# Optimization experiments

Hardware: AMD Instinct MI355X
Metric: run time of the kernel (lower is better)

## Reference

```python
import jax, jax.numpy as jnp
import numpy as np

B, S, D = 2, 4096, 512   # batch, seq_len, input_dim
W, H = 256, 4            # memory width (d_model), attention heads
DH = W // H              # per-head depth


def _dense(x, w, b):
    return x @ w + b


def setup_inputs() -> dict:
    key = jax.random.key(0)
    ks = jax.random.split(key, 24)
    def w(k, shape):
        return jax.random.normal(k, shape, dtype=jnp.float32) * 0.02
    inp = {
        "x": jax.random.normal(ks[0], (B, S, D), dtype=jnp.float32),
        # outer q/k/v projections D -> W
        "qp_w": w(ks[1], (D, W)), "qp_b": jnp.zeros((W,), jnp.float32),
        "kp_w": w(ks[2], (D, W)), "kp_b": jnp.zeros((W,), jnp.float32),
        "vp_w": w(ks[3], (D, W)), "vp_b": jnp.zeros((W,), jnp.float32),
        # MHA internal projections W -> W
        "wq_w": w(ks[4], (W, W)), "wq_b": jnp.zeros((W,), jnp.float32),
        "wk_w": w(ks[5], (W, W)), "wk_b": jnp.zeros((W,), jnp.float32),
        "wv_w": w(ks[6], (W, W)), "wv_b": jnp.zeros((W,), jnp.float32),
        "wo_w": w(ks[7], (W, W)), "wo_b": jnp.zeros((W,), jnp.float32),
        # deep MLP memory (depth=2, gelu) + its output proj W -> W
        "m0_w": w(ks[8], (W, W)), "m0_b": jnp.zeros((W,), jnp.float32),
        "m1_w": w(ks[9], (W, W)), "m1_b": jnp.zeros((W,), jnp.float32),
        "mo_w": w(ks[10], (W, W)), "mo_b": jnp.zeros((W,), jnp.float32),
        # final output projection W -> D
        "op_w": w(ks[11], (W, D)), "op_b": jnp.zeros((D,), jnp.float32),
    }
    return inp


def reference(x, qp_w, qp_b, kp_w, kp_b, vp_w, vp_b,
              wq_w, wq_b, wk_w, wk_b, wv_w, wv_b, wo_w, wo_b,
              m0_w, m0_b, m1_w, m1_b, mo_w, mo_b, op_w, op_b):
    # outer projections (D -> W)
    q0 = _dense(x, qp_w, qp_b)
    k0 = _dense(x, kp_w, kp_b)
    v0 = _dense(x, vp_w, vp_b)
    # MHA internal projections (W -> W)
    q = _dense(q0, wq_w, wq_b)
    k = _dense(k0, wk_w, wk_b)
    v = _dense(v0, wv_w, wv_b)
    # split heads: [B,S,W] -> [B,H,S,DH]
    def split(t):
        return t.reshape(B, S, H, DH).transpose(0, 2, 1, 3)
    qh, kh, vh = split(q), split(k), split(v)
    scores = jnp.einsum('bhqd,bhkd->bhqk', qh, kh) / jnp.sqrt(jnp.float32(DH))
    attn = jax.nn.softmax(scores, axis=-1)
    ctx = jnp.einsum('bhqk,bhkd->bhqd', attn, vh)
    ctx = ctx.transpose(0, 2, 1, 3).reshape(B, S, W)
    retrieved = _dense(ctx, wo_w, wo_b)
    # deep MLP memory (exact gelu, matching keras 'gelu')
    h = jax.nn.gelu(_dense(retrieved, m0_w, m0_b), approximate=False)
    h = jax.nn.gelu(_dense(h, m1_w, m1_b), approximate=False)
    mem = _dense(h, mo_w, mo_b)
    # final projection + residual
    out = _dense(mem, op_w, op_b) + x
    return out
```

## Files before the change

### kernel.cpp

```cpp
#include <hip/hip_runtime.h>
#include <cstdint>
#include <cstddef>


#define GAS(p) ((const __attribute__((address_space(1))) void*)(p))
#define LAS(p) ((__attribute__((address_space(3))) void*)(p))

typedef __attribute__((ext_vector_type(8))) short bfrag;
typedef __attribute__((ext_vector_type(4))) float facc;
typedef __attribute__((ext_vector_type(16))) float facc16;
typedef uint16_t u16;

__device__ __forceinline__ u16 f2bf(float f) {
  uint32_t u = __float_as_uint(f);
  u += 0x7fffu + ((u >> 16) & 1u);
  return (u16)(u >> 16);
}
__device__ __forceinline__ float bf2f(u16 h) {
  return __uint_as_float((uint32_t)h << 16);
}
__device__ __forceinline__ float gelu_exact(float v) {
  return 0.5f * v * (1.f + erff(v * 0.70710678118654752440f));
}
__device__ __forceinline__ facc mfma16(bfrag a, bfrag b, facc c) {
  return __builtin_amdgcn_mfma_f32_16x16x32_bf16(a, b, c, 0, 0, 0);
}
__device__ __forceinline__ facc16 mfma32(bfrag a, bfrag b, facc16 c) {
  return __builtin_amdgcn_mfma_f32_32x32x16_bf16(a, b, c, 0, 0, 0);
}

union U4 { uint32_t w[4]; bfrag f; };

__device__ __forceinline__ bfrag lds_frag(const u16* lds, int row, int kk, int ln) {
  int kb  = (kk << 6) + ((ln >> 4) << 4);
  int off = (row << 7) + (kb ^ ((row & 7) << 4));
  return *(const bfrag*)((const char*)lds + off);
}
__device__ __forceinline__ bfrag lds_frag_rb(const u16* lds, int row, int bytecol) {
  int off = (row << 7) + (bytecol ^ ((row & 7) << 4));
  return *(const bfrag*)((const char*)lds + off);
}

template <int ROWS, int NW>
__device__ __forceinline__ void stage_tile(const u16* gbase, int ldK, u16* lds,
                                           int wv, int ln) {
#pragma unroll
  for (int i = 0; i < ROWS / 8 / NW; i++) {
    int seg = i * NW + wv;
    int row = (seg << 3) + (ln >> 3);
    int kb  = (ln & 7) << 4;
    const char* g = (const char*)(gbase + (size_t)row * ldK) +
                    (kb ^ ((row & 7) << 4));
    __builtin_amdgcn_global_load_lds(GAS(g), LAS(lds + (seg << 9)), 16, 0, 0);
  }
}

template <int EPI, int BN>
__global__ __launch_bounds__(256) void gemm_bt(
    const u16* __restrict__ A, const u16* __restrict__ Bt,
    const float* __restrict__ bias, const float* __restrict__ resid,
    u16* __restrict__ obf, float* __restrict__ of32,
    u16* __restrict__ qb, u16* __restrict__ kb2, u16* __restrict__ vb,
    int M, int N, int K) {
  const int t = threadIdx.x, wv = t >> 6, ln = t & 63;
  const int wr = wv >> 1, wc = wv & 1;
  const int m0 = blockIdx.y << 7, n0 = blockIdx.x * BN;
  constexpr int NJ = BN / 32;

  __shared__ __align__(16) u16 Al[128 * 64];
  __shared__ __align__(16) u16 Bl[BN * 64];

  facc acc[4][NJ];
#pragma unroll
  for (int i = 0; i < 4; i++)
#pragma unroll
    for (int j = 0; j < NJ; j++)
#pragma unroll
      for (int r = 0; r < 4; r++) acc[i][j][r] = 0.f;

  const u16* Ab = A + (size_t)m0 * K;
  const u16* Bb = Bt + (size_t)n0 * K;
  stage_tile<128, 4>(Ab, K, Al, wv, ln);
  stage_tile<BN, 4>(Bb, K, Bl, wv, ln);

  const int nk = K >> 6;
  for (int kt = 0; kt < nk; ++kt) {
    __syncthreads();
#pragma unroll
    for (int kk = 0; kk < 2; kk++) {
      bfrag av[4], bv[NJ];
#pragma unroll
      for (int i = 0; i < 4; i++)
        av[i] = lds_frag(Al, (wr << 6) + (i << 4) + (ln & 15), kk, ln);
#pragma unroll
      for (int j = 0; j < NJ; j++)
        bv[j] = lds_frag(Bl, wc * (BN / 2) + (j << 4) + (ln & 15), kk, ln);
      __builtin_amdgcn_s_setprio(1);
#pragma unroll
      for (int i = 0; i < 4; i++)
#pragma unroll
        for (int j = 0; j < NJ; j++)
          acc[i][j] = mfma16(av[i], bv[j], acc[i][j]);
      __builtin_amdgcn_s_setprio(0);
    }
    if (kt + 1 < nk) {
      __syncthreads();
      stage_tile<128, 4>(Ab + (kt + 1) * 64, K, Al, wv, ln);
      stage_tile<BN, 4>(Bb + (kt + 1) * 64, K, Bl, wv, ln);
    }
  }

  const int rb = (ln >> 4) << 2, cb = ln & 15;
#pragma unroll
  for (int i = 0; i < 4; i++) {
#pragma unroll
    for (int j = 0; j < NJ; j++) {
      const int col = n0 + wc * (BN / 2) + (j << 4) + cb;
      const float bcol = bias ? bias[col] : 0.f;
#pragma unroll
      for (int r = 0; r < 4; r++) {
        const int row = m0 + (wr << 6) + (i << 4) + rb + r;
        float val = acc[i][j][r] + bcol;
        if (EPI == 0) {
          obf[(size_t)row * N + col] = f2bf(val);
        } else if (EPI == 1) {
          obf[(size_t)row * N + col] = f2bf(gelu_exact(val));
        } else if (EPI == 2) {
          const int sec = col >> 8, cc = col & 255, h = cc >> 6, dh = cc & 63;
          const int b = row >> 12, s = row & 4095;
          const size_t idx = (((size_t)(b * 4 + h)) * 4096 + s) * 64 + dh;
          if (sec == 0) qb[idx] = f2bf(val * 0.18033688011112042f);
          else if (sec == 1) kb2[idx] = f2bf(val);
          else vb[idx] = f2bf(val);
        } else {
          of32[(size_t)row * N + col] = val + resid[(size_t)row * N + col];
        }
      }
    }
  }
}

__global__ __launch_bounds__(256) void wgemm5(
    const u16* __restrict__ wqkvT, const u16* __restrict__ owqkv,
    const u16* __restrict__ m0_t, const u16* __restrict__ wo_bf,
    const u16* __restrict__ opT, const u16* __restrict__ mo_bf,
    u16* __restrict__ Wqkv_t, u16* __restrict__ Wf1_t,
    u16* __restrict__ Wmo_t) {
  const int z = blockIdx.z;
  const u16 *A, *Bt; u16* out; int M, N, rowOff;
  if (z < 3)      { A = wqkvT + z * 65536; Bt = owqkv + z * 131072;
                    out = Wqkv_t; M = 256; N = 512; rowOff = z * 256; }
  else if (z == 3){ A = m0_t; Bt = wo_bf; out = Wf1_t; M = 256; N = 256; rowOff = 0; }
  else            { A = opT;  Bt = mo_bf; out = Wmo_t; M = 512; N = 256; rowOff = 0; }
  const int m0 = blockIdx.y << 7, n0 = blockIdx.x << 6;
  if (m0 >= M || n0 >= N) return;

  const int t = threadIdx.x, wv = t >> 6, ln = t & 63;
  const int wr = wv >> 1, wc = wv & 1;
  __shared__ __align__(16) u16 Al[128 * 64];
  __shared__ __align__(16) u16 Bl[64 * 64];

  facc acc[4][2];
#pragma unroll
  for (int i = 0; i < 4; i++)
#pragma unroll
    for (int j = 0; j < 2; j++)
#pragma unroll
      for (int r = 0; r < 4; r++) acc[i][j][r] = 0.f;

  const u16* Ab = A + (size_t)m0 * 256;
  const u16* Bb = Bt + (size_t)n0 * 256;
  stage_tile<128, 4>(Ab, 256, Al, wv, ln);
  stage_tile<64, 4>(Bb, 256, Bl, wv, ln);

  for (int kt = 0; kt < 4; ++kt) {
    __syncthreads();
#pragma unroll
    for (int kk = 0; kk < 2; kk++) {
      bfrag av[4], bv[2];
#pragma unroll
      for (int i = 0; i < 4; i++)
        av[i] = lds_frag(Al, (wr << 6) + (i << 4) + (ln & 15), kk, ln);
#pragma unroll
      for (int j = 0; j < 2; j++)
        bv[j] = lds_frag(Bl, wc * 32 + (j << 4) + (ln & 15), kk, ln);
#pragma unroll
      for (int i = 0; i < 4; i++)
#pragma unroll
        for (int j = 0; j < 2; j++)
          acc[i][j] = mfma16(av[i], bv[j], acc[i][j]);
    }
    if (kt + 1 < 4) {
      __syncthreads();
      stage_tile<128, 4>(Ab + (kt + 1) * 64, 256, Al, wv, ln);
      stage_tile<64, 4>(Bb + (kt + 1) * 64, 256, Bl, wv, ln);
    }
  }

  const int rb = (ln >> 4) << 2, cb = ln & 15;
#pragma unroll
  for (int i = 0; i < 4; i++)
#pragma unroll
    for (int j = 0; j < 2; j++) {
      const int col = n0 + wc * 32 + (j << 4) + cb;
#pragma unroll
      for (int r = 0; r < 4; r++) {
        const int row = m0 + (wr << 6) + (i << 4) + rb + r;
        out[(size_t)(rowOff + row) * N + col] = f2bf(acc[i][j][r]);
      }
    }
}

__global__ __launch_bounds__(128) void attn4(
    const u16* __restrict__ qg, const u16* __restrict__ kg,
    const u16* __restrict__ vtg, u16* __restrict__ Opart,
    float* __restrict__ lpart) {
  const int t = threadIdx.x, wv = t >> 6, ln = t & 63;
  const int l31 = ln & 31, lh = ln >> 5;
  const int qt = blockIdx.x, bh = blockIdx.y, kv = blockIdx.z;
  const int qbase = qt * 128 + wv * 64;
  const u16* Q  = qg + ((size_t)bh * 4096 + qbase) * 64;
  const u16* Kb = kg + ((size_t)bh * 4096 + kv * 1024) * 64;
  const u16* Vt = vtg + (size_t)bh * 64 * 4096 + kv * 1024;

  __shared__ __align__(16) u16 Klds[2][4096];
  __shared__ __align__(16) u16 Vlds[2][4096];

  bfrag qf[2][4];
#pragma unroll
  for (int qi = 0; qi < 2; qi++) {
    const u16* qp = Q + (size_t)(((qi << 5) + l31) << 6) + (lh << 3);
#pragma unroll
    for (int dc = 0; dc < 4; dc++)
      qf[qi][dc] = *(const bfrag*)(qp + (dc << 4));
  }
  bfrag ones;
#pragma unroll
  for (int j = 0; j < 8; j++) ones[j] = (short)0x3F80;

  facc16 oacc[2][2];
  facc16 lacc[2];
#pragma unroll
  for (int qi = 0; qi < 2; qi++) {
#pragma unroll
    for (int r = 0; r < 16; r++) {
      oacc[qi][0][r] = 0.f; oacc[qi][1][r] = 0.f; lacc[qi][r] = 0.f;
    }
  }

  stage_tile<64, 2>(Kb, 64, Klds[0], wv, ln);
  stage_tile<64, 2>(Vt, 4096, Vlds[0], wv, ln);

  for (int kt = 0; kt < 16; ++kt) {
    const int cur = kt & 1;
    __syncthreads();
    if (kt < 15) {
      stage_tile<64, 2>(Kb + (size_t)(kt + 1) * 64 * 64, 64, Klds[cur ^ 1], wv, ln);
      stage_tile<64, 2>(Vt + (kt + 1) * 64, 4096, Vlds[cur ^ 1], wv, ln);
    }
#pragma unroll
    for (int kb = 0; kb < 2; kb++) {
      bfrag kf[4];
#pragma unroll
      for (int dc = 0; dc < 4; dc++)
        kf[dc] = lds_frag_rb(Klds[cur], (kb << 5) + l31, (dc << 5) + (lh << 4));

      bfrag pa[2][2];
#pragma unroll
      for (int qi = 0; qi < 2; qi++) {
        facc16 sa;
#pragma unroll
        for (int r = 0; r < 16; r++) sa[r] = 0.f;
        __builtin_amdgcn_s_setprio(1);
#pragma unroll
        for (int dc = 0; dc < 4; dc++)
          sa = mfma32(kf[dc], qf[qi][dc], sa);
        __builtin_amdgcn_s_setprio(0);
        float p[16];
#pragma unroll
        for (int r = 0; r < 16; r++) p[r] = exp2f(sa[r]);
        uint32_t u0, u1, u2, u3, u4, u5, u6, u7;
        asm("v_cvt_pk_bf16_f32 %0, %1, %2" : "=v"(u0) : "v"(p[0]),  "v"(p[1]));
        asm("v_cvt_pk_bf16_f32 %0, %1, %2" : "=v"(u1) : "v"(p[2]),  "v"(p[3]));
        asm("v_cvt_pk_bf16_f32 %0, %1, %2" : "=v"(u2) : "v"(p[4]),  "v"(p[5]));
        asm("v_cvt_pk_bf16_f32 %0, %1, %2" : "=v"(u3) : "v"(p[6]),  "v"(p[7]));
        asm("v_cvt_pk_bf16_f32 %0, %1, %2" : "=v"(u4) : "v"(p[8]),  "v"(p[9]));
        asm("v_cvt_pk_bf16_f32 %0, %1, %2" : "=v"(u5) : "v"(p[10]), "v"(p[11]));
        asm("v_cvt_pk_bf16_f32 %0, %1, %2" : "=v"(u6) : "v"(p[12]), "v"(p[13]));
        asm("v_cvt_pk_bf16_f32 %0, %1, %2" : "=v"(u7) : "v"(p[14]), "v"(p[15]));
        asm volatile("v_permlane32_swap_b32 %0, %1" : "+v"(u0), "+v"(u2));
        asm volatile("v_permlane32_swap_b32 %0, %1" : "+v"(u1), "+v"(u3));
        asm volatile("v_permlane32_swap_b32 %0, %1" : "+v"(u4), "+v"(u6));
        asm volatile("v_permlane32_swap_b32 %0, %1" : "+v"(u5), "+v"(u7));
        U4 c0; c0.w[0] = u0; c0.w[1] = u1; c0.w[2] = u2; c0.w[3] = u3;
        U4 c1; c1.w[0] = u4; c1.w[1] = u5; c1.w[2] = u6; c1.w[3] = u7;
        pa[qi][0] = c0.f;
        pa[qi][1] = c1.f;
      }
#pragma unroll
      for (int c = 0; c < 2; c++) {
        bfrag vf0 = lds_frag_rb(Vlds[cur], l31,
                                (kb << 6) + (c << 5) + (lh << 4));
        bfrag vf1 = lds_frag_rb(Vlds[cur], 32 + l31,
                                (kb << 6) + (c << 5) + (lh << 4));
        __builtin_amdgcn_s_setprio(1);
        oacc[0][0] = mfma32(pa[0][c], vf0, oacc[0][0]);
        oacc[1][0] = mfma32(pa[1][c], vf0, oacc[1][0]);
        oacc[0][1] = mfma32(pa[0][c], vf1, oacc[0][1]);
        oacc[1][1] = mfma32(pa[1][c], vf1, oacc[1][1]);
        lacc[0] = mfma32(pa[0][c], ones, lacc[0]);
        lacc[1] = mfma32(pa[1][c], ones, lacc[1]);
        __builtin_amdgcn_s_setprio(0);
      }
    }
  }

  const size_t obase = (size_t)(kv * 8 + bh) * 4096 + qbase;
#pragma unroll
  for (int qi = 0; qi < 2; qi++) {
#pragma unroll
    for (int r = 0; r < 16; r++) {
      const int qrow = (qi << 5) + (r & 3) + ((r >> 2) << 3) + (lh << 2);
#pragma unroll
      for (int dj = 0; dj < 2; dj++)
        Opart[(obase + qrow) * 64 + (dj << 5) + l31] = f2bf(oacc[qi][dj][r]);
      if (l31 == 0) lpart[obase + qrow] = lacc[qi][r];
    }
  }
}

__global__ __launch_bounds__(256) void attn_combine4(
    const u16* __restrict__ Opart, const float* __restrict__ lpart,
    u16* __restrict__ ctx) {
  const int idx = blockIdx.x * 256 + threadIdx.x;
  const int d0 = (idx & 7) << 3, s = (idx >> 3) & 4095, bh = idx >> 15;
  const size_t sb = (size_t)bh * 4096 + s;
  float acc[8] = {0.f, 0.f, 0.f, 0.f, 0.f, 0.f, 0.f, 0.f};
  float lsum = 0.f;
#pragma unroll
  for (int pz = 0; pz < 4; pz++) {
    const size_t pb = (size_t)pz * 8 * 4096;
    bfrag a = *(const bfrag*)(Opart + (pb + sb) * 64 + d0);
#pragma unroll
    for (int j = 0; j < 8; j++) acc[j] += bf2f((u16)a[j]);
    lsum += lpart[pb + sb];
  }
  const float rl = 1.f / lsum;
  bfrag o;
#pragma unroll
  for (int j = 0; j < 8; j++) o[j] = (short)f2bf(acc[j] * rl);
  *(bfrag*)(ctx + ((size_t)(bh >> 2) * 4096 + s) * 256 + ((bh & 3) << 6) + d0) = o;
}

__global__ __launch_bounds__(256) void prep_all(
    const float* __restrict__ x,
    const float* __restrict__ qp, const float* __restrict__ kp,
    const float* __restrict__ vp, const float* __restrict__ mo,
    const float* __restrict__ wo,
    const float* __restrict__ wq, const float* __restrict__ wk,
    const float* __restrict__ wv, const float* __restrict__ m0,
    const float* __restrict__ m1, const float* __restrict__ op_w,
    const float* __restrict__ qp_b, const float* __restrict__ kp_b,
    const float* __restrict__ vp_b, const float* __restrict__ wq_b,
    const float* __restrict__ wk_b, const float* __restrict__ wv_b,
    const float* __restrict__ mo_b, const float* __restrict__ op_b,
    const float* __restrict__ wo_b, const float* __restrict__ m0_b,
    u16* __restrict__ xb, u16* __restrict__ owqkv, u16* __restrict__ mo_bf,
    u16* __restrict__ wo_bf, u16* __restrict__ wqkvT, u16* __restrict__ m0_t,
    u16* __restrict__ m1_t, u16* __restrict__ opT,
    float* __restrict__ bqkv, float* __restrict__ bmo,
    float* __restrict__ bf1) {
  const int bid = blockIdx.x, t = threadIdx.x;
  if (bid < 2048) {
    const size_t i = ((size_t)bid * 256 + t) * 8;
    float4 a = *(const float4*)(x + i);
    float4 b = *(const float4*)(x + i + 4);
    bfrag o;
    o[0] = (short)f2bf(a.x); o[1] = (short)f2bf(a.y);
    o[2] = (short)f2bf(a.z); o[3] = (short)f2bf(a.w);
    o[4] = (short)f2bf(b.x); o[5] = (short)f2bf(b.y);
    o[6] = (short)f2bf(b.z); o[7] = (short)f2bf(b.w);
    *(bfrag*)(xb + i) = o;
  } else if (bid < 2176) {
    const int i = (bid - 2048) * 4096 + t * 16;
    const float* s; u16* dst; int off;
    if (i < 131072)      { s = qp; dst = owqkv;          off = i; }
    else if (i < 262144) { s = kp; dst = owqkv + 131072; off = i - 131072; }
    else if (i < 393216) { s = vp; dst = owqkv + 262144; off = i - 262144; }
    else if (i < 458752) { s = mo; dst = mo_bf;          off = i - 393216; }
    else                 { s = wo; dst = wo_bf;          off = i - 458752; }
    bfrag o0, o1;
#pragma unroll
    for (int q = 0; q < 2; q++) {
      float4 v0 = *(const float4*)(s + off + q * 8);
      float4 v1 = *(const float4*)(s + off + q * 8 + 4);
      bfrag& o = q ? o1 : o0;
      o[0] = (short)f2bf(v0.x); o[1] = (short)f2bf(v0.y);
      o[2] = (short)f2bf(v0.z); o[3] = (short)f2bf(v0.w);
      o[4] = (short)f2bf(v1.x); o[5] = (short)f2bf(v1.y);
      o[6] = (short)f2bf(v1.z); o[7] = (short)f2bf(v1.w);
    }
    *(bfrag*)(dst + off) = o0;
    *(bfrag*)(dst + off + 8) = o1;
  } else if (bid < 2288) {
    __shared__ float tile[64][65];
    const int tid = bid - 2176;
    const float* src; u16* dst; int r0, c0, ldS, ldD;
    if (tid < 80) {
      const int mi = tid >> 4, tt = tid & 15;
      r0 = ((tt >> 2) << 6); c0 = ((tt & 3) << 6); ldS = 256; ldD = 256;
      switch (mi) {
        case 0: src = wq; dst = wqkvT; break;
        case 1: src = wk; dst = wqkvT + 65536; break;
        case 2: src = wv; dst = wqkvT + 131072; break;
        case 3: src = m0; dst = m0_t; break;
        default: src = m1; dst = m1_t; break;
      }
    } else {
      const int tt = tid - 80;
      r0 = ((tt >> 3) << 6); c0 = ((tt & 7) << 6);
      ldS = 512; ldD = 256; src = op_w; dst = opT;
    }
    {
      const int r = t >> 2, cc = (t & 3) << 4;
      const float* sp = src + (size_t)(r0 + r) * ldS + c0 + cc;
#pragma unroll
      for (int q = 0; q < 4; q++) {
        float4 v = *(const float4*)(sp + q * 4);
        tile[r][cc + q * 4 + 0] = v.x; tile[r][cc + q * 4 + 1] = v.y;
        tile[r][cc + q * 4 + 2] = v.z; tile[r][cc + q * 4 + 3] = v.w;
      }
    }
    __syncthreads();
    {
      const int cl = t >> 2, k16 = (t & 3) << 4;
      bfrag o0, o1;
#pragma unroll
      for (int j = 0; j < 8; j++) {
        o0[j] = (short)f2bf(tile[k16 + j][cl]);
        o1[j] = (short)f2bf(tile[k16 + 8 + j][cl]);
      }
      u16* dp = dst + (size_t)(c0 + cl) * ldD + r0 + k16;
      *(bfrag*)(dp) = o0;
      *(bfrag*)(dp + 8) = o1;
    }
  } else {
    const int bz = bid - 2288;
    if (bz < 3) {
      const float* ob = bz == 0 ? qp_b : (bz == 1 ? kp_b : vp_b);
      const float* iw = bz == 0 ? wq : (bz == 1 ? wk : wv);
      const float* ib = bz == 0 ? wq_b : (bz == 1 ? wk_b : wv_b);
      float s = 0.f;
      for (int c = 0; c < 256; c++) s += ob[c] * iw[(size_t)c * 256 + t];
      bqkv[bz * 256 + t] = s + ib[t];
    } else if (bz < 5) {
      const int d = (bz - 3) * 256 + t;
      float s = 0.f;
      for (int c = 0; c < 256; c++) s += mo_b[c] * op_w[(size_t)c * 512 + d];
      bmo[d] = s + op_b[d];
    } else {
      float s = 0.f;
      for (int c = 0; c < 256; c++) s += wo_b[c] * m0[(size_t)c * 256 + t];
      bf1[t] = s + m0_b[t];
    }
  }
}

__global__ __launch_bounds__(256) void transpose_v(const u16* __restrict__ v,
                                                   u16* __restrict__ vt) {
  const int bh = blockIdx.x >> 6, st = blockIdx.x & 63, t = threadIdx.x;
  __shared__ u16 tile[64][65];
  const u16* src = v + ((size_t)bh * 4096 + st * 64) * 64;
  {
    const int r = t >> 2, c0 = (t & 3) << 4;
    bfrag x0 = *(const bfrag*)(src + (size_t)r * 64 + c0);
    bfrag x1 = *(const bfrag*)(src + (size_t)r * 64 + c0 + 8);
#pragma unroll
    for (int j = 0; j < 8; j++) {
      tile[r][c0 + j] = (u16)x0[j];
      tile[r][c0 + 8 + j] = (u16)x1[j];
    }
  }
  __syncthreads();
  {
    const int d = t >> 2, s0 = (t & 3) << 4;
    bfrag y0, y1;
#pragma unroll
    for (int j = 0; j < 8; j++) {
      y0[j] = (short)tile[s0 + j][d];
      y1[j] = (short)tile[s0 + 8 + j][d];
    }
    u16* dst = vt + ((size_t)bh * 64 + d) * 4096 + (st << 6) + s0;
    *(bfrag*)(dst) = y0;
    *(bfrag*)(dst + 8) = y1;
  }
}

extern "C" void kernel_launch(void* const* d_in, const int* in_sizes, int n_in,
                              void* d_out, int out_size, void* d_ws,
                              size_t ws_size, hipStream_t stream) {
  const float* x    = (const float*)d_in[0];
  const float* qp_w = (const float*)d_in[1];
  const float* qp_b = (const float*)d_in[2];
  const float* kp_w = (const float*)d_in[3];
  const float* kp_b = (const float*)d_in[4];
  const float* vp_w = (const float*)d_in[5];
  const float* vp_b = (const float*)d_in[6];
  const float* wq_w = (const float*)d_in[7];
  const float* wq_b = (const float*)d_in[8];
  const float* wk_w = (const float*)d_in[9];
  const float* wk_b = (const float*)d_in[10];
  const float* wv_w = (const float*)d_in[11];
  const float* wv_b = (const float*)d_in[12];
  const float* wo_w = (const float*)d_in[13];
  const float* wo_b = (const float*)d_in[14];
  const float* m0_w = (const float*)d_in[15];
  const float* m0_b = (const float*)d_in[16];
  const float* m1_w = (const float*)d_in[17];
  const float* m1_b = (const float*)d_in[18];
  const float* mo_w = (const float*)d_in[19];
  const float* mo_b = (const float*)d_in[20];
  const float* op_w = (const float*)d_in[21];
  const float* op_b = (const float*)d_in[22];
  float* out = (float*)d_out;

  char* ws = (char*)d_ws;
  u16*   xb     = (u16*)(ws);
  u16*   v_buf  = (u16*)(ws + 8388608);
  u16*   Opart  = (u16*)(ws);
  u16*   q_buf  = (u16*)(ws + 16777216);
  u16*   k_buf  = (u16*)(ws + 20971520);
  u16*   vt_buf = (u16*)(ws + 25165824);
  u16*   ctx    = (u16*)(ws + 29360128);
  float* lpart  = (float*)(ws + 33554432);
  u16*   owqkv  = (u16*)(ws + 34078720);
  u16*   wqkvT  = (u16*)(ws + 34865152);
  u16*   Wqkv_t = (u16*)(ws + 35258368);
  u16*   m0_t   = (u16*)(ws + 36044800);
  u16*   m1_t   = (u16*)(ws + 36175872);
  u16*   opT    = (u16*)(ws + 36306944);
  u16*   mo_bf  = (u16*)(ws + 36569088);
  u16*   wo_bf  = (u16*)(ws + 36700160);
  u16*   Wf1_t  = (u16*)(ws + 36831232);
  u16*   Wmo_t  = (u16*)(ws + 36962304);
  float* bqkv   = (float*)(ws + 37224448);
  float* bmo    = (float*)(ws + 37227520);
  float* bf1    = (float*)(ws + 37229568);
  u16* h1 = q_buf;
  u16* h2 = k_buf;

  prep_all<<<2294, 256, 0, stream>>>(
      x, qp_w, kp_w, vp_w, mo_w, wo_w,
      wq_w, wk_w, wv_w, m0_w, m1_w, op_w,
      qp_b, kp_b, vp_b, wq_b, wk_b, wv_b, mo_b, op_b, wo_b, m0_b,
      xb, owqkv, mo_bf, wo_bf, wqkvT, m0_t, m1_t, opT, bqkv, bmo, bf1);
  wgemm5<<<dim3(8, 4, 5), 256, 0, stream>>>(
      wqkvT, owqkv, m0_t, wo_bf, opT, mo_bf, Wqkv_t, Wf1_t, Wmo_t);

  gemm_bt<2, 128><<<dim3(6, 64), 256, 0, stream>>>(
      xb, Wqkv_t, bqkv, nullptr, nullptr, nullptr, q_buf, k_buf, v_buf,
      8192, 768, 512);
  transpose_v<<<512, 256, 0, stream>>>(v_buf, vt_buf);
  attn4<<<dim3(32, 8, 4), 128, 0, stream>>>(q_buf, k_buf, vt_buf, Opart, lpart);
  attn_combine4<<<1024, 256, 0, stream>>>(Opart, lpart, ctx);

  gemm_bt<1, 64><<<dim3(4, 64), 256, 0, stream>>>(
      ctx, Wf1_t, bf1, nullptr, h1, nullptr, nullptr, nullptr, nullptr,
      8192, 256, 256);
  gemm_bt<1, 64><<<dim3(4, 64), 256, 0, stream>>>(
      h1, m1_t, m1_b, nullptr, h2, nullptr, nullptr, nullptr, nullptr,
      8192, 256, 256);
  gemm_bt<3, 128><<<dim3(4, 64), 256, 0, stream>>>(
      h2, Wmo_t, bmo, x, nullptr, out, nullptr, nullptr, nullptr,
      8192, 512, 256);
}
```

Baseline: 247.7 us.

## Write K/V directly in MFMA fragment layout and drop V transpose kernel

The QKV GEMM epilogue now scatters K and V straight into per-32-key fragment-ordered tiles, so the separate transpose_v kernel is removed. The attention kernel loads those tiles with contiguous global-to-LDS copies and reads fragments without swizzling. It processes 32 keys per step, computes row sums with VALU adds instead of ones-matrix MFMAs, and can use more KV splits when the workspace allows. The scattered epilogue writes may coalesce poorly, and the QKV GEMM tile width is halved. Workspace offsets are reorganized to match.

```diff
diff --git a/kernel.cpp b/kernel.cpp
--- a/kernel.cpp
+++ b/kernel.cpp
@@ -34,10 +34,6 @@
 __device__ __forceinline__ bfrag lds_frag(const u16* lds, int row, int kk, int ln) {
   int kb  = (kk << 6) + ((ln >> 4) << 4);
   int off = (row << 7) + (kb ^ ((row & 7) << 4));
-  return *(const bfrag*)((const char*)lds + off);
-}
-__device__ __forceinline__ bfrag lds_frag_rb(const u16* lds, int row, int bytecol) {
-  int off = (row << 7) + (bytecol ^ ((row & 7) << 4));
   return *(const bfrag*)((const char*)lds + off);
 }
 
@@ -128,10 +124,22 @@
         } else if (EPI == 2) {
           const int sec = col >> 8, cc = col & 255, h = cc >> 6, dh = cc & 63;
           const int b = row >> 12, s = row & 4095;
-          const size_t idx = (((size_t)(b * 4 + h)) * 4096 + s) * 64 + dh;
-          if (sec == 0) qb[idx] = f2bf(val * 0.18033688011112042f);
-          else if (sec == 1) kb2[idx] = f2bf(val);
-          else vb[idx] = f2bf(val);
+          const int bh = b * 4 + h;
+          if (sec == 0) {
+            qb[((size_t)bh * 4096 + s) * 64 + dh] =
+                f2bf(val * 0.18033688011112042f);
+          } else if (sec == 1) {
+            const int kt2 = s >> 5, kl = s & 31;
+            const int dc = dh >> 4, lane = kl + ((dh >> 3) & 1) * 32, e = dh & 7;
+            kb2[((size_t)bh * 128 + kt2) * 2048 + dc * 512 + lane * 8 + e] =
+                f2bf(val);
+          } else {
+            const int kt2 = s >> 5, c = (s >> 4) & 1;
+            const int lane = ((s >> 3) & 1) * 32 + (dh & 31), e = s & 7;
+            const int dj = dh >> 5;
+            vb[((size_t)bh * 128 + kt2) * 2048 + (c * 2 + dj) * 512 +
+               lane * 8 + e] = f2bf(val);
+          }
         } else {
           of32[(size_t)row * N + col] = val + resid[(size_t)row * N + col];
         }
@@ -211,20 +219,20 @@
     }
 }
 
-__global__ __launch_bounds__(128) void attn4(
-    const u16* __restrict__ qg, const u16* __restrict__ kg,
-    const u16* __restrict__ vtg, u16* __restrict__ Opart,
-    float* __restrict__ lpart) {
+__global__ __launch_bounds__(128, 4) void attn5(
+    const u16* __restrict__ qg, const u16* __restrict__ kfg,
+    const u16* __restrict__ vfg, u16* __restrict__ Opart,
+    float* __restrict__ lpart, int NT) {
   const int t = threadIdx.x, wv = t >> 6, ln = t & 63;
   const int l31 = ln & 31, lh = ln >> 5;
   const int qt = blockIdx.x, bh = blockIdx.y, kv = blockIdx.z;
   const int qbase = qt * 128 + wv * 64;
   const u16* Q  = qg + ((size_t)bh * 4096 + qbase) * 64;
-  const u16* Kb = kg + ((size_t)bh * 4096 + kv * 1024) * 64;
-  const u16* Vt = vtg + (size_t)bh * 64 * 4096 + kv * 1024;
-
-  __shared__ __align__(16) u16 Klds[2][4096];
-  __shared__ __align__(16) u16 Vlds[2][4096];
+  const u16* Kf = kfg + ((size_t)bh * 128 + (size_t)kv * NT) * 2048;
+  const u16* Vf = vfg + ((size_t)bh * 128 + (size_t)kv * NT) * 2048;
+
+  __shared__ __align__(16) u16 Klds[2][2048];
+  __shared__ __align__(16) u16 Vlds[2][2048];
 
   bfrag qf[2][4];
 #pragma unroll
@@ -234,88 +242,90 @@
     for (int dc = 0; dc < 4; dc++)
       qf[qi][dc] = *(const bfrag*)(qp + (dc << 4));
   }
-  bfrag ones;
-#pragma unroll
-  for (int j = 0; j < 8; j++) ones[j] = (short)0x3F80;
 
   facc16 oacc[2][2];
-  facc16 lacc[2];
-#pragma unroll
-  for (int qi = 0; qi < 2; qi++) {
-#pragma unroll
-    for (int r = 0; r < 16; r++) {
-      oacc[qi][0][r] = 0.f; oacc[qi][1][r] = 0.f; lacc[qi][r] = 0.f;
-    }
-  }
-
-  stage_tile<64, 2>(Kb, 64, Klds[0], wv, ln);
-  stage_tile<64, 2>(Vt, 4096, Vlds[0], wv, ln);
-
-  for (int kt = 0; kt < 16; ++kt) {
+#pragma unroll
+  for (int qi = 0; qi < 2; qi++)
+#pragma unroll
+    for (int r = 0; r < 16; r++) { oacc[qi][0][r] = 0.f; oacc[qi][1][r] = 0.f; }
+  float lsum0 = 0.f, lsum1 = 0.f;
+
+  {
+    const u16* src = wv ? Vf : Kf;
+    u16* dst = wv ? Vlds[0] : Klds[0];
+#pragma unroll
+    for (int i = 0; i < 4; i++)
+      __builtin_amdgcn_global_load_lds(GAS(src + i * 512 + ln * 8),
+                                       LAS(dst + i * 512), 16, 0, 0);
+  }
+
+  for (int kt = 0; kt < NT; ++kt) {
     const int cur = kt & 1;
     __syncthreads();
-    if (kt < 15) {
-      stage_tile<64, 2>(Kb + (size_t)(kt + 1) * 64 * 64, 64, Klds[cur ^ 1], wv, ln);
-      stage_tile<64, 2>(Vt + (kt + 1) * 64, 4096, Vlds[cur ^ 1], wv, ln);
-    }
-#pragma unroll
-    for (int kb = 0; kb < 2; kb++) {
-      bfrag kf[4];
+    if (kt + 1 < NT) {
+      const u16* src = (wv ? Vf : Kf) + (size_t)(kt + 1) * 2048;
+      u16* dst = wv ? Vlds[cur ^ 1] : Klds[cur ^ 1];
+#pragma unroll
+      for (int i = 0; i < 4; i++)
+        __builtin_amdgcn_global_load_lds(GAS(src + i * 512 + ln * 8),
+                                         LAS(dst + i * 512), 16, 0, 0);
+    }
+    bfrag kf[4];
+#pragma unroll
+    for (int dc = 0; dc < 4; dc++)
+      kf[dc] = *(const bfrag*)(Klds[cur] + dc * 512 + ln * 8);
+
+    bfrag pa[2][2];
+#pragma unroll
+    for (int qi = 0; qi < 2; qi++) {
+      facc16 sa;
+#pragma unroll
+      for (int r = 0; r < 16; r++) sa[r] = 0.f;
+      __builtin_amdgcn_s_setprio(1);
 #pragma unroll
       for (int dc = 0; dc < 4; dc++)
-        kf[dc] = lds_frag_rb(Klds[cur], (kb << 5) + l31, (dc << 5) + (lh << 4));
-
-      bfrag pa[2][2];
-#pragma unroll
-      for (int qi = 0; qi < 2; qi++) {
-        facc16 sa;
-#pragma unroll
-        for (int r = 0; r < 16; r++) sa[r] = 0.f;
-        __builtin_amdgcn_s_setprio(1);
-#pragma unroll
-        for (int dc = 0; dc < 4; dc++)
-          sa = mfma32(kf[dc], qf[qi][dc], sa);
-        __builtin_amdgcn_s_setprio(0);
-        float p[16];
-#pragma unroll
-        for (int r = 0; r < 16; r++) p[r] = exp2f(sa[r]);
-        uint32_t u0, u1, u2, u3, u4, u5, u6, u7;
-        asm("v_cvt_pk_bf16_f32 %0, %1, %2" : "=v"(u0) : "v"(p[0]),  "v"(p[1]));
-        asm("v_cvt_pk_bf16_f32 %0, %1, %2" : "=v"(u1) : "v"(p[2]),  "v"(p[3]));
-        asm("v_cvt_pk_bf16_f32 %0, %1, %2" : "=v"(u2) : "v"(p[4]),  "v"(p[5]));
-        asm("v_cvt_pk_bf16_f32 %0, %1, %2" : "=v"(u3) : "v"(p[6]),  "v"(p[7]));
-        asm("v_cvt_pk_bf16_f32 %0, %1, %2" : "=v"(u4) : "v"(p[8]),  "v"(p[9]));
-        asm("v_cvt_pk_bf16_f32 %0, %1, %2" : "=v"(u5) : "v"(p[10]), "v"(p[11]));
-        asm("v_cvt_pk_bf16_f32 %0, %1, %2" : "=v"(u6) : "v"(p[12]), "v"(p[13]));
-        asm("v_cvt_pk_bf16_f32 %0, %1, %2" : "=v"(u7) : "v"(p[14]), "v"(p[15]));
-        asm volatile("v_permlane32_swap_b32 %0, %1" : "+v"(u0), "+v"(u2));
-        asm volatile("v_permlane32_swap_b32 %0, %1" : "+v"(u1), "+v"(u3));
-        asm volatile("v_permlane32_swap_b32 %0, %1" : "+v"(u4), "+v"(u6));
-        asm volatile("v_permlane32_swap_b32 %0, %1" : "+v"(u5), "+v"(u7));
-        U4 c0; c0.w[0] = u0; c0.w[1] = u1; c0.w[2] = u2; c0.w[3] = u3;
-        U4 c1; c1.w[0] = u4; c1.w[1] = u5; c1.w[2] = u6; c1.w[3] = u7;
-        pa[qi][0] = c0.f;
-        pa[qi][1] = c1.f;
-      }
-#pragma unroll
-      for (int c = 0; c < 2; c++) {
-        bfrag vf0 = lds_frag_rb(Vlds[cur], l31,
-                                (kb << 6) + (c << 5) + (lh << 4));
-        bfrag vf1 = lds_frag_rb(Vlds[cur], 32 + l31,
-                                (kb << 6) + (c << 5) + (lh << 4));
-        __builtin_amdgcn_s_setprio(1);
-        oacc[0][0] = mfma32(pa[0][c], vf0, oacc[0][0]);
-        oacc[1][0] = mfma32(pa[1][c], vf0, oacc[1][0]);
-        oacc[0][1] = mfma32(pa[0][c], vf1, oacc[0][1]);
-        oacc[1][1] = mfma32(pa[1][c], vf1, oacc[1][1]);
-        lacc[0] = mfma32(pa[0][c], ones, lacc[0]);
-        lacc[1] = mfma32(pa[1][c], ones, lacc[1]);
-        __builtin_amdgcn_s_setprio(0);
-      }
-    }
-  }
-
-  const size_t obase = (size_t)(kv * 8 + bh) * 4096 + qbase;
+        sa = mfma32(kf[dc], qf[qi][dc], sa);
+      __builtin_amdgcn_s_setprio(0);
+      float p[16];
+      float ls = 0.f;
+#pragma unroll
+      for (int r = 0; r < 16; r++) { p[r] = exp2f(sa[r]); ls += p[r]; }
+      if (qi == 0) lsum0 += ls; else lsum1 += ls;
+      uint32_t u0, u1, u2, u3, u4, u5, u6, u7;
+      asm("v_cvt_pk_bf16_f32 %0, %1, %2" : "=v"(u0) : "v"(p[0]),  "v"(p[1]));
+      asm("v_cvt_pk_bf16_f32 %0, %1, %2" : "=v"(u1) : "v"(p[2]),  "v"(p[3]));
+      asm("v_cvt_pk_bf16_f32 %0, %1, %2" : "=v"(u2) : "v"(p[4]),  "v"(p[5]));
+      asm("v_cvt_pk_bf16_f32 %0, %1, %2" : "=v"(u3) : "v"(p[6]),  "v"(p[7]));
+      asm("v_cvt_pk_bf16_f32 %0, %1, %2" : "=v"(u4) : "v"(p[8]),  "v"(p[9]));
+      asm("v_cvt_pk_bf16_f32 %0, %1, %2" : "=v"(u5) : "v"(p[10]), "v"(p[11]));
+      asm("v_cvt_pk_bf16_f32 %0, %1, %2" : "=v"(u6) : "v"(p[12]), "v"(p[13]));
+      asm("v_cvt_pk_bf16_f32 %0, %1, %2" : "=v"(u7) : "v"(p[14]), "v"(p[15]));
+      asm volatile("v_permlane32_swap_b32 %0, %1" : "+v"(u0), "+v"(u2));
+      asm volatile("v_permlane32_swap_b32 %0, %1" : "+v"(u1), "+v"(u3));
+      asm volatile("v_permlane32_swap_b32 %0, %1" : "+v"(u4), "+v"(u6));
+      asm volatile("v_permlane32_swap_b32 %0, %1" : "+v"(u5), "+v"(u7));
+      U4 c0; c0.w[0] = u0; c0.w[1] = u1; c0.w[2] = u2; c0.w[3] = u3;
+      U4 c1; c1.w[0] = u4; c1.w[1] = u5; c1.w[2] = u6; c1.w[3] = u7;
+      pa[qi][0] = c0.f;
+      pa[qi][1] = c1.f;
+    }
+#pragma unroll
+    for (int c = 0; c < 2; c++) {
+      bfrag vf0 = *(const bfrag*)(Vlds[cur] + (c * 2 + 0) * 512 + ln * 8);
+      bfrag vf1 = *(const bfrag*)(Vlds[cur] + (c * 2 + 1) * 512 + ln * 8);
+      __builtin_amdgcn_s_setprio(1);
+      oacc[0][0] = mfma32(pa[0][c], vf0, oacc[0][0]);
+      oacc[1][0] = mfma32(pa[1][c], vf0, oacc[1][0]);
+      oacc[0][1] = mfma32(pa[0][c], vf1, oacc[0][1]);
+      oacc[1][1] = mfma32(pa[1][c], vf1, oacc[1][1]);
+      __builtin_amdgcn_s_setprio(0);
+    }
+  }
+
+  lsum0 += __shfl_xor(lsum0, 32);
+  lsum1 += __shfl_xor(lsum1, 32);
+
+  const size_t obase = ((size_t)kv * 8 + bh) * 4096 + qbase;
 #pragma unroll
   for (int qi = 0; qi < 2; qi++) {
 #pragma unroll
@@ -324,21 +334,21 @@
 #pragma unroll
       for (int dj = 0; dj < 2; dj++)
         Opart[(obase + qrow) * 64 + (dj << 5) + l31] = f2bf(oacc[qi][dj][r]);
-      if (l31 == 0) lpart[obase + qrow] = lacc[qi][r];
-    }
-  }
-}
-
-__global__ __launch_bounds__(256) void attn_combine4(
+    }
+    if (lh == 0)
+      lpart[obase + (qi << 5) + l31] = qi == 0 ? lsum0 : lsum1;
+  }
+}
+
+__global__ __launch_bounds__(256) void attn_combineN(
     const u16* __restrict__ Opart, const float* __restrict__ lpart,
-    u16* __restrict__ ctx) {
+    u16* __restrict__ ctx, int np) {
   const int idx = blockIdx.x * 256 + threadIdx.x;
   const int d0 = (idx & 7) << 3, s = (idx >> 3) & 4095, bh = idx >> 15;
   const size_t sb = (size_t)bh * 4096 + s;
   float acc[8] = {0.f, 0.f, 0.f, 0.f, 0.f, 0.f, 0.f, 0.f};
   float lsum = 0.f;
-#pragma unroll
-  for (int pz = 0; pz < 4; pz++) {
+  for (int pz = 0; pz < np; pz++) {
     const size_t pb = (size_t)pz * 8 * 4096;
     bfrag a = *(const bfrag*)(Opart + (pb + sb) * 64 + d0);
 #pragma unroll
@@ -466,36 +476,6 @@
   }
 }
 
-__global__ __launch_bounds__(256) void transpose_v(const u16* __restrict__ v,
-                                                   u16* __restrict__ vt) {
-  const int bh = blockIdx.x >> 6, st = blockIdx.x & 63, t = threadIdx.x;
-  __shared__ u16 tile[64][65];
-  const u16* src = v + ((size_t)bh * 4096 + st * 64) * 64;
-  {
-    const int r = t >> 2, c0 = (t & 3) << 4;
-    bfrag x0 = *(const bfrag*)(src + (size_t)r * 64 + c0);
-    bfrag x1 = *(const bfrag*)(src + (size_t)r * 64 + c0 + 8);
-#pragma unroll
-    for (int j = 0; j < 8; j++) {
-      tile[r][c0 + j] = (u16)x0[j];
-      tile[r][c0 + 8 + j] = (u16)x1[j];
-    }
-  }
-  __syncthreads();
-  {
-    const int d = t >> 2, s0 = (t & 3) << 4;
-    bfrag y0, y1;
-#pragma unroll
-    for (int j = 0; j < 8; j++) {
-      y0[j] = (short)tile[s0 + j][d];
-      y1[j] = (short)tile[s0 + 8 + j][d];
-    }
-    u16* dst = vt + ((size_t)bh * 64 + d) * 4096 + (st << 6) + s0;
-    *(bfrag*)(dst) = y0;
-    *(bfrag*)(dst + 8) = y1;
-  }
-}
-
 extern "C" void kernel_launch(void* const* d_in, const int* in_sizes, int n_in,
                               void* d_out, int out_size, void* d_ws,
                               size_t ws_size, hipStream_t stream) {
@@ -524,30 +504,34 @@
   const float* op_b = (const float*)d_in[22];
   float* out = (float*)d_out;
 
+  const size_t MB = 1024 * 1024;
+  const int kvs = (ws_size >= 56 * MB) ? 8 : 4;
+  const int NT = 128 / kvs;
+
   char* ws = (char*)d_ws;
-  u16*   xb     = (u16*)(ws);
-  u16*   v_buf  = (u16*)(ws + 8388608);
-  u16*   Opart  = (u16*)(ws);
-  u16*   q_buf  = (u16*)(ws + 16777216);
-  u16*   k_buf  = (u16*)(ws + 20971520);
-  u16*   vt_buf = (u16*)(ws + 25165824);
-  u16*   ctx    = (u16*)(ws + 29360128);
-  float* lpart  = (float*)(ws + 33554432);
-  u16*   owqkv  = (u16*)(ws + 34078720);
-  u16*   wqkvT  = (u16*)(ws + 34865152);
-  u16*   Wqkv_t = (u16*)(ws + 35258368);
-  u16*   m0_t   = (u16*)(ws + 36044800);
-  u16*   m1_t   = (u16*)(ws + 36175872);
-  u16*   opT    = (u16*)(ws + 36306944);
-  u16*   mo_bf  = (u16*)(ws + 36569088);
-  u16*   wo_bf  = (u16*)(ws + 36700160);
-  u16*   Wf1_t  = (u16*)(ws + 36831232);
-  u16*   Wmo_t  = (u16*)(ws + 36962304);
-  float* bqkv   = (float*)(ws + 37224448);
-  float* bmo    = (float*)(ws + 37227520);
-  float* bf1    = (float*)(ws + 37229568);
+  u16*   q_buf  = (u16*)(ws);
+  u16*   kf_buf = (u16*)(ws + 4 * MB);
+  u16*   vf_buf = (u16*)(ws + 8 * MB);
+  u16*   ctx    = (u16*)(ws + 12 * MB);
+  u16*   xb     = (u16*)(ws + 16 * MB);
+  u16*   Opart  = (u16*)(ws + 16 * MB);
+  char*  wb     = ws + 16 * MB + (size_t)kvs * 4 * MB;
+  u16*   owqkv  = (u16*)(wb);
+  u16*   wqkvT  = (u16*)(wb + 786432);
+  u16*   Wqkv_t = (u16*)(wb + 1179648);
+  u16*   m0_t   = (u16*)(wb + 1966080);
+  u16*   m1_t   = (u16*)(wb + 2097152);
+  u16*   opT    = (u16*)(wb + 2228224);
+  u16*   mo_bf  = (u16*)(wb + 2490368);
+  u16*   wo_bf  = (u16*)(wb + 2621440);
+  u16*   Wf1_t  = (u16*)(wb + 2752512);
+  u16*   Wmo_t  = (u16*)(wb + 2883584);
+  float* bqkv   = (float*)(wb + 3145728);
+  float* bmo    = (float*)(wb + 3149824);
+  float* bf1    = (float*)(wb + 3151872);
+  float* lpart  = (float*)(wb + 3153920);
   u16* h1 = q_buf;
-  u16* h2 = k_buf;
+  u16* h2 = kf_buf;
 
   prep_all<<<2294, 256, 0, stream>>>(
       x, qp_w, kp_w, vp_w, mo_w, wo_w,
@@ -557,12 +541,12 @@
   wgemm5<<<dim3(8, 4, 5), 256, 0, stream>>>(
       wqkvT, owqkv, m0_t, wo_bf, opT, mo_bf, Wqkv_t, Wf1_t, Wmo_t);
 
-  gemm_bt<2, 128><<<dim3(6, 64), 256, 0, stream>>>(
-      xb, Wqkv_t, bqkv, nullptr, nullptr, nullptr, q_buf, k_buf, v_buf,
+  gemm_bt<2, 64><<<dim3(12, 64), 256, 0, stream>>>(
+      xb, Wqkv_t, bqkv, nullptr, nullptr, nullptr, q_buf, kf_buf, vf_buf,
       8192, 768, 512);
-  transpose_v<<<512, 256, 0, stream>>>(v_buf, vt_buf);
-  attn4<<<dim3(32, 8, 4), 128, 0, stream>>>(q_buf, k_buf, vt_buf, Opart, lpart);
-  attn_combine4<<<1024, 256, 0, stream>>>(Opart, lpart, ctx);
+  attn5<<<dim3(32, 8, kvs), 128, 0, stream>>>(q_buf, kf_buf, vf_buf,
+                                              Opart, lpart, NT);
+  attn_combineN<<<1024, 256, 0, stream>>>(Opart, lpart, ctx, kvs);
 
   gemm_bt<1, 64><<<dim3(4, 64), 256, 0, stream>>>(
       ctx, Wf1_t, bf1, nullptr, h1, nullptr, nullptr, nullptr, nullptr,
```

After: 357.0 us. +44.2%, slower.
